# Kernel optimization log

Measured on AMD Instinct MI355X. Metric: run time of the kernel, lower is better.

## Reference

```python
import jax, jax.numpy as jnp
import numpy as np

N, E, B = 8000, 128000, 16
DIN, D, H, C, L = 16, 256, 8, 32, 6
MC, NT = 200, 8
NEG_SLOPE = 0.2


def layernorm(x, s, b):
    mu = jnp.mean(x, axis=-1, keepdims=True)
    var = jnp.mean(jnp.square(x - mu), axis=-1, keepdims=True)
    return (x - mu) * jax.lax.rsqrt(var + 1e-5) * s + b


def setup_inputs() -> dict:
    key = jax.random.key(0)
    ks = iter(jax.random.split(key, 64))
    rn = lambda shape, s=0.05: jax.random.normal(next(ks), shape, jnp.float32) * s
    inp = {}
    inp['x'] = jax.random.normal(next(ks), (N, DIN), jnp.float32)
    inp['edge_index'] = jax.random.randint(next(ks), (2, E), 0, N)
    inp['batch'] = jnp.sort(jax.random.randint(next(ks), (N,), 0, B))
    # node encoder: Linear(DIN,D) + LayerNorm
    inp['enc_W'] = rn((DIN, D)); inp['enc_b'] = jnp.zeros((D,), jnp.float32)
    inp['enc_ls'] = jnp.ones((D,), jnp.float32); inp['enc_lb'] = jnp.zeros((D,), jnp.float32)
    # GATv2 layers (stacked): lin_l, lin_r, att, output bias, post LayerNorm
    inp['Wl'] = rn((L, D, D)); inp['bl'] = jnp.zeros((L, D), jnp.float32)
    inp['Wr'] = rn((L, D, D)); inp['br'] = jnp.zeros((L, D), jnp.float32)
    inp['att'] = rn((L, H, C))
    inp['gb'] = jnp.zeros((L, D), jnp.float32)
    inp['gls'] = jnp.ones((L, D), jnp.float32); inp['glb'] = jnp.zeros((L, D), jnp.float32)
    # color head MLP: D -> D -> D//2 -> MC
    inp['cW1'] = rn((D, D)); inp['cb1'] = jnp.zeros((D,), jnp.float32)
    inp['cW2'] = rn((D, D // 2)); inp['cb2'] = jnp.zeros((D // 2,), jnp.float32)
    inp['cW3'] = rn((D // 2, MC)); inp['cb3'] = jnp.zeros((MC,), jnp.float32)
    # chromatic head: 2D -> D -> D//2 -> MC
    inp['chW1'] = rn((2 * D, D)); inp['chb1'] = jnp.zeros((D,), jnp.float32)
    inp['chW2'] = rn((D, D // 2)); inp['chb2'] = jnp.zeros((D // 2,), jnp.float32)
    inp['chW3'] = rn((D // 2, MC)); inp['chb3'] = jnp.zeros((MC,), jnp.float32)
    # type head: 2D -> 128 -> NT
    inp['tW1'] = rn((2 * D, 128)); inp['tb1'] = jnp.zeros((128,), jnp.float32)
    inp['tW2'] = rn((128, NT)); inp['tb2'] = jnp.zeros((NT,), jnp.float32)
    # difficulty head: 2D -> 64 -> 1, sigmoid * 100
    inp['dW1'] = rn((2 * D, 64)); inp['db1'] = jnp.zeros((64,), jnp.float32)
    inp['dW2'] = rn((64, 1)); inp['db2'] = jnp.zeros((1,), jnp.float32)
    return inp


def reference(x, edge_index, batch, enc_W, enc_b, enc_ls, enc_lb,
              Wl, bl, Wr, br, att, gb, gls, glb,
              cW1, cb1, cW2, cb2, cW3, cb3,
              chW1, chb1, chW2, chb2, chW3, chb3,
              tW1, tb1, tW2, tb2, dW1, db1, dW2, db2):
    n = x.shape[0]
    # node encoder (dropout = identity at inference)
    h = jax.nn.relu(layernorm(x @ enc_W + enc_b, enc_ls, enc_lb))
    # add self loops once (same for every layer)
    sl = jnp.arange(n)
    src = jnp.concatenate([edge_index[0], sl])  # message source j
    dst = jnp.concatenate([edge_index[1], sl])  # message target i
    for i in range(L):
        xl = (h @ Wl[i] + bl[i]).reshape(n, H, C)  # source transform
        xr = (h @ Wr[i] + br[i]).reshape(n, H, C)  # target transform
        # GATv2 attention: a^T LeakyReLU(xl_j + xr_i)
        e = jax.nn.leaky_relu(xl[src] + xr[dst], NEG_SLOPE)  # [E+N, H, C]
        logits = jnp.einsum('ehc,hc->eh', e, att[i])          # [E+N, H]
        # segment softmax over destination node (self-loops guarantee denom > 0)
        m = jax.ops.segment_max(logits, dst, num_segments=n)
        m = jnp.where(jnp.isfinite(m), m, 0.0)
        p = jnp.exp(logits - m[dst])
        denom = jax.ops.segment_sum(p, dst, num_segments=n)
        alpha = p / denom[dst]
        out = jax.ops.segment_sum(xl[src] * alpha[:, :, None], dst, num_segments=n)
        out = out.reshape(n, D) + gb[i]
        h_new = jax.nn.elu(layernorm(out, gls[i], glb[i]))
        h = h + h_new if i > 0 else h_new
    # per-node color logits
    z = jax.nn.relu(h @ cW1 + cb1)
    z = jax.nn.relu(z @ cW2 + cb2)
    node_colors = z @ cW3 + cb3
    # global mean/max pooling per graph
    cnt = jax.ops.segment_sum(jnp.ones((n,), h.dtype), batch, num_segments=B)
    mean_p = jax.ops.segment_sum(h, batch, num_segments=B) / jnp.maximum(cnt, 1.0)[:, None]
    max_p = jax.ops.segment_max(h, batch, num_segments=B)
    max_p = jnp.where(jnp.isfinite(max_p), max_p, 0.0)
    g = jnp.concatenate([mean_p, max_p], axis=1)  # [B, 2D]
    zc = jax.nn.relu(g @ chW1 + chb1)
    zc = jax.nn.relu(zc @ chW2 + chb2)
    chromatic_num = zc @ chW3 + chb3
    zt = jax.nn.relu(g @ tW1 + tb1)
    graph_type = zt @ tW2 + tb2
    zd = jax.nn.relu(g @ dW1 + db1)
    difficulty = jax.nn.sigmoid(zd @ dW2 + db2) * 100.0
    return (node_colors, chromatic_num, graph_type, difficulty)
```

## Files before the change

### kernel.cpp

```cpp
#include <hip/hip_runtime.h>
#include <hip/hip_bf16.h>

constexpr int DIN = 16;
constexpr int D   = 256;
constexpr int NH  = 8;
constexpr int NC  = 32;
constexpr int MC  = 200;
constexpr int NT  = 8;
constexpr int BG  = 16;
constexpr int NL  = 6;
constexpr int PS  = 16;
constexpr float NEG = 0.2f;

typedef __attribute__((ext_vector_type(8))) short bfrag;
typedef __attribute__((ext_vector_type(4))) float f32x4;

__device__ inline unsigned short f2bf(float f) {
    unsigned int u = __float_as_uint(f);
    u += 0x7FFFu + ((u >> 16) & 1u);
    return (unsigned short)(u >> 16);
}
__device__ inline float bf2f(unsigned short u) {
    return __uint_as_float((unsigned int)u << 16);
}

__device__ inline float dot_ilp(const float* __restrict__ g, const float* __restrict__ W,
                                int K, int ldw, int t) {
    float a0 = 0.f, a1 = 0.f, a2 = 0.f, a3 = 0.f;
    for (int k = 0; k < K; k += 4) {
        a0 = fmaf(g[k + 0], W[(k + 0) * ldw + t], a0);
        a1 = fmaf(g[k + 1], W[(k + 1) * ldw + t], a1);
        a2 = fmaf(g[k + 2], W[(k + 2) * ldw + t], a2);
        a3 = fmaf(g[k + 3], W[(k + 3) * ldw + t], a3);
    }
    return (a0 + a1) + (a2 + a3);
}

__global__ __launch_bounds__(256) void init_k(int* __restrict__ deg, int N) {
    int i = blockIdx.x * 256 + threadIdx.x;
    if (i < N) deg[i] = 1;
}

__global__ __launch_bounds__(256) void enc_k(const float* __restrict__ x, const float* __restrict__ W,
                                             const float* __restrict__ b, const float* __restrict__ ls,
                                             const float* __restrict__ lb, float* __restrict__ h, int N) {
    int t = threadIdx.x;
    int lane = t & 63;
    int n = blockIdx.x * 4 + (t >> 6);
    if (n >= N) return;
    int c4 = lane * 4;
    float xs[DIN];
#pragma unroll
    for (int k = 0; k < DIN; k += 4) {
        float4 xv = *(const float4*)&x[n * DIN + k];
        xs[k] = xv.x; xs[k + 1] = xv.y; xs[k + 2] = xv.z; xs[k + 3] = xv.w;
    }
    float4 a = *(const float4*)&b[c4];
#pragma unroll
    for (int k = 0; k < DIN; k++) {
        float4 wv = *(const float4*)&W[k * D + c4];
        a.x = fmaf(xs[k], wv.x, a.x);
        a.y = fmaf(xs[k], wv.y, a.y);
        a.z = fmaf(xs[k], wv.z, a.z);
        a.w = fmaf(xs[k], wv.w, a.w);
    }
    float s = a.x + a.y + a.z + a.w;
#pragma unroll
    for (int msk = 1; msk <= 32; msk <<= 1) s += __shfl_xor(s, msk);
    float mu = s * (1.f / D);
    float4 dv = make_float4(a.x - mu, a.y - mu, a.z - mu, a.w - mu);
    float v2 = dv.x * dv.x + dv.y * dv.y + dv.z * dv.z + dv.w * dv.w;
#pragma unroll
    for (int msk = 1; msk <= 32; msk <<= 1) v2 += __shfl_xor(v2, msk);
    float rstd = rsqrtf(v2 * (1.f / D) + 1e-5f);
    float4 lsv = *(const float4*)&ls[c4];
    float4 lbv = *(const float4*)&lb[c4];
    float4 y = make_float4(fmaxf(dv.x * rstd * lsv.x + lbv.x, 0.f),
                           fmaxf(dv.y * rstd * lsv.y + lbv.y, 0.f),
                           fmaxf(dv.z * rstd * lsv.z + lbv.z, 0.f),
                           fmaxf(dv.w * rstd * lsv.w + lbv.w, 0.f));
    *(float4*)&h[(size_t)n * D + c4] = y;
}

__global__ __launch_bounds__(256) void count_k(const int* __restrict__ dst, int* __restrict__ deg, int E) {
    int e = blockIdx.x * 256 + threadIdx.x;
    if (e < E) atomicAdd(&deg[dst[e]], 1);
}

__global__ __launch_bounds__(1024) void scan_k(const int* __restrict__ deg, int* __restrict__ row_ptr,
                                               int* __restrict__ fill, int N) {
    __shared__ int sd[1024];
    int t = threadIdx.x;
    int chunk = (N + 1023) >> 10;
    int lo = t * chunk, hi = min(lo + chunk, N);
    int s = 0;
    for (int i = lo; i < hi; i++) s += deg[i];
    sd[t] = s;
    __syncthreads();
    for (int off = 1; off < 1024; off <<= 1) {
        int v = (t >= off) ? sd[t - off] : 0;
        __syncthreads();
        sd[t] += v;
        __syncthreads();
    }
    int run = (t > 0) ? sd[t - 1] : 0;
    for (int i = lo; i < hi; i++) {
        row_ptr[i] = run; fill[i] = run;
        run += deg[i];
    }
    if (t == 1023) row_ptr[N] = sd[1023];
}

__global__ __launch_bounds__(256) void scatter_k(const int* __restrict__ src, const int* __restrict__ dst,
                                                 int* __restrict__ fill, int* __restrict__ col, int E, int N) {
    int e = blockIdx.x * 256 + threadIdx.x;
    if (e < E) {
        int p = atomicAdd(&fill[dst[e]], 1);
        col[p] = src[e];
    } else if (e < E + N) {
        int n = e - E;
        int p = atomicAdd(&fill[n], 1);
        col[p] = n;
    }
}

__global__ __launch_bounds__(256) void repack_k(const float* __restrict__ Wl, const float* __restrict__ Wr,
                                                unsigned short* __restrict__ Wp) {
    int tid = blockIdx.x * 256 + threadIdx.x;
    int lane = tid & 63;
    int r1 = tid >> 6;
    int ks = r1 & 7;
    int r2 = r1 >> 3;
    int ct = r2 & 15;
    int mi = r2 >> 4;
    int layer = mi >> 1, mat = mi & 1;
    const float* W = (mat == 0 ? Wl : Wr) + (size_t)layer * D * D;
    int n = ct * 16 + (lane & 15);
    int kb = ks * 32 + (lane >> 4) * 8;
    size_t base = (((size_t)(mi * 16 + ct) * 8 + ks) * 64 + lane) * 8;
#pragma unroll
    for (int j = 0; j < 8; j++) Wp[base + j] = f2bf(W[(size_t)(kb + j) * D + n]);
}

__global__ __launch_bounds__(256) void repack_c(const float* __restrict__ W, unsigned short* __restrict__ Wp,
                                                int K, int NCOL, int nct, int nks) {
    int tid = blockIdx.x * 256 + threadIdx.x;
    int total = nct * nks * 64;
    if (tid >= total) return;
    int lane = tid & 63;
    int r = tid >> 6;
    int ks = r % nks;
    int ct = r / nks;
    int n = ct * 16 + (lane & 15);
    int kb = ks * 32 + (lane >> 4) * 8;
    size_t base = (((size_t)ct * nks + ks) * 64 + lane) * 8;
#pragma unroll
    for (int j = 0; j < 8; j++) {
        int k = kb + j;
        Wp[base + j] = (n < NCOL && k < K) ? f2bf(W[(size_t)k * NCOL + n]) : (unsigned short)0;
    }
}

__global__ __launch_bounds__(256) void gemm_mfma_k(const float* __restrict__ h,
                                                   const unsigned short* __restrict__ WpL,
                                                   const unsigned short* __restrict__ WpR,
                                                   const float* __restrict__ bl, const float* __restrict__ br,
                                                   unsigned short* __restrict__ xl, unsigned short* __restrict__ xr,
                                                   int N) {
    int t = threadIdx.x;
    int lane = t & 63;
    int w = t >> 6;
    int nb = blockIdx.x * 16;
    __shared__ unsigned short As[16][264];
#pragma unroll
    for (int r = 0; r < 16; r++) {
        int row = nb + r;
        float v = (row < N) ? h[(size_t)row * D + t] : 0.f;
        As[r][t] = f2bf(v);
    }
    __syncthreads();
    int m = lane & 15;
    int q = lane >> 4;
    int ctbase = w * 4;
    f32x4 accL[4], accR[4];
#pragma unroll
    for (int ct = 0; ct < 4; ct++) {
        float bLv = bl[(ctbase + ct) * 16 + m];
        float bRv = br[(ctbase + ct) * 16 + m];
        accL[ct] = (f32x4){bLv, bLv, bLv, bLv};
        accR[ct] = (f32x4){bRv, bRv, bRv, bRv};
    }
#pragma unroll 2
    for (int ks = 0; ks < 8; ks++) {
        bfrag af = *(const bfrag*)&As[m][ks * 32 + q * 8];
#pragma unroll
        for (int ct = 0; ct < 4; ct++) {
            int ctg = ctbase + ct;
            size_t off = (((size_t)ctg * 8 + ks) * 64 + lane) * 8;
            bfrag bL = *(const bfrag*)&WpL[off];
            bfrag bR = *(const bfrag*)&WpR[off];
            accL[ct] = __builtin_amdgcn_mfma_f32_16x16x32_bf16(af, bL, accL[ct], 0, 0, 0);
            accR[ct] = __builtin_amdgcn_mfma_f32_16x16x32_bf16(af, bR, accR[ct], 0, 0, 0);
        }
    }
#pragma unroll
    for (int ct = 0; ct < 4; ct++) {
        int colg = (ctbase + ct) * 16 + m;
#pragma unroll
        for (int reg = 0; reg < 4; reg++) {
            int row = nb + q * 4 + reg;
            if (row < N) {
                xl[(size_t)row * D + colg] = f2bf(accL[ct][reg]);
                xr[(size_t)row * D + colg] = f2bf(accR[ct][reg]);
            }
        }
    }
}

__global__ __launch_bounds__(256) void attn_k(const unsigned short* __restrict__ xl,
                                              const unsigned short* __restrict__ xr,
                                              const int* __restrict__ row_ptr, const int* __restrict__ col,
                                              const float* __restrict__ att, const float* __restrict__ gb,
                                              const float* __restrict__ gls, const float* __restrict__ glb,
                                              float* __restrict__ h, int layer, int N) {
    int t = threadIdx.x;
    int lane = t & 63;
    int n = blockIdx.x * 4 + (t >> 6);
    if (n >= N) return;
    int c4 = lane * 4;
    ushort4 xr4 = *(const ushort4*)&xr[(size_t)n * D + c4];
    float4 xrv = make_float4(bf2f(xr4.x), bf2f(xr4.y), bf2f(xr4.z), bf2f(xr4.w));
    float4 av  = *(const float4*)&att[c4];
    int beg = row_ptr[n], end = row_ptr[n + 1];
    int deg = end - beg;
    int myc = col[beg + min(lane, deg - 1)];

    float m = -3.0e38f, l = 0.f;
    float4 acc = make_float4(0.f, 0.f, 0.f, 0.f);

    auto loadx = [&](int i) -> ushort4 {
        if (i < deg) {
            int s = (i < 64) ? __shfl(myc, i) : col[beg + i];
            return *(const ushort4*)&xl[(size_t)s * D + c4];
        }
        return make_ushort4(0, 0, 0, 0);
    };
    auto step = [&](ushort4 x4) {
        float4 xlv = make_float4(bf2f(x4.x), bf2f(x4.y), bf2f(x4.z), bf2f(x4.w));
        float sx = xlv.x + xrv.x; sx = sx > 0.f ? sx : NEG * sx;
        float sy = xlv.y + xrv.y; sy = sy > 0.f ? sy : NEG * sy;
        float sz = xlv.z + xrv.z; sz = sz > 0.f ? sz : NEG * sz;
        float sw = xlv.w + xrv.w; sw = sw > 0.f ? sw : NEG * sw;
        float z = av.x * sx + av.y * sy + av.z * sz + av.w * sw;
        z += __shfl_xor(z, 1); z += __shfl_xor(z, 2); z += __shfl_xor(z, 4);
        float mn = fmaxf(m, z);
        float sc = __expf(m - mn);
        float p  = __expf(z - mn);
        l = l * sc + p;
        acc.x = acc.x * sc + p * xlv.x;
        acc.y = acc.y * sc + p * xlv.y;
        acc.z = acc.z * sc + p * xlv.z;
        acc.w = acc.w * sc + p * xlv.w;
        m = mn;
    };

    ushort4 b0 = loadx(0), b1 = loadx(1), b2 = loadx(2), b3 = loadx(3);
    int e = 0;
    for (; e + 4 <= deg; e += 4) {
        ushort4 n0 = loadx(e + 4), n1 = loadx(e + 5), n2 = loadx(e + 6), n3 = loadx(e + 7);
        step(b0); step(b1); step(b2); step(b3);
        b0 = n0; b1 = n1; b2 = n2; b3 = n3;
    }
    if (e + 0 < deg) step(b0);
    if (e + 1 < deg) step(b1);
    if (e + 2 < deg) step(b2);

    float4 gbv  = *(const float4*)&gb[c4];
    float rl = 1.f / l;
    float4 o = make_float4(acc.x * rl + gbv.x, acc.y * rl + gbv.y,
                           acc.z * rl + gbv.z, acc.w * rl + gbv.w);
    float s = o.x + o.y + o.z + o.w;
#pragma unroll
    for (int msk = 1; msk <= 32; msk <<= 1) s += __shfl_xor(s, msk);
    float mu = s * (1.f / D);
    float4 dv = make_float4(o.x - mu, o.y - mu, o.z - mu, o.w - mu);
    float v2 = dv.x * dv.x + dv.y * dv.y + dv.z * dv.z + dv.w * dv.w;
#pragma unroll
    for (int msk = 1; msk <= 32; msk <<= 1) v2 += __shfl_xor(v2, msk);
    float rstd = rsqrtf(v2 * (1.f / D) + 1e-5f);
    float4 glsv = *(const float4*)&gls[c4];
    float4 glbv = *(const float4*)&glb[c4];
    float y0 = dv.x * rstd * glsv.x + glbv.x;
    float y1 = dv.y * rstd * glsv.y + glbv.y;
    float y2 = dv.z * rstd * glsv.z + glbv.z;
    float y3 = dv.w * rstd * glsv.w + glbv.w;
    y0 = y0 > 0.f ? y0 : expm1f(y0);
    y1 = y1 > 0.f ? y1 : expm1f(y1);
    y2 = y2 > 0.f ? y2 : expm1f(y2);
    y3 = y3 > 0.f ? y3 : expm1f(y3);
    float4 prev = make_float4(0.f, 0.f, 0.f, 0.f);
    if (layer > 0) prev = *(const float4*)&h[(size_t)n * D + c4];
    float4 res = make_float4(prev.x + y0, prev.y + y1, prev.z + y2, prev.w + y3);
    *(float4*)&h[(size_t)n * D + c4] = res;
}

__global__ __launch_bounds__(256) void color_mfma_k(const float* __restrict__ h,
                                                    const unsigned short* __restrict__ W1p, const float* __restrict__ b1,
                                                    const unsigned short* __restrict__ W2p, const float* __restrict__ b2,
                                                    const unsigned short* __restrict__ W3p, const float* __restrict__ b3,
                                                    float* __restrict__ out, int N) {
    int t = threadIdx.x;
    int lane = t & 63;
    int w = t >> 6;
    int nb = blockIdx.x * 16;
    __shared__ unsigned short As[16][264];
    __shared__ unsigned short Zs[16][264];
#pragma unroll
    for (int r = 0; r < 16; r++) {
        int row = nb + r;
        float v = (row < N) ? h[(size_t)row * D + t] : 0.f;
        As[r][t] = f2bf(v);
    }
    __syncthreads();
    int m = lane & 15;
    int q = lane >> 4;
    {
        f32x4 acc[4];
#pragma unroll
        for (int ct = 0; ct < 4; ct++) {
            float bv = b1[(w * 4 + ct) * 16 + m];
            acc[ct] = (f32x4){bv, bv, bv, bv};
        }
#pragma unroll 2
        for (int ks = 0; ks < 8; ks++) {
            bfrag af = *(const bfrag*)&As[m][ks * 32 + q * 8];
#pragma unroll
            for (int ct = 0; ct < 4; ct++) {
                int ctg = w * 4 + ct;
                bfrag bf = *(const bfrag*)&W1p[(((size_t)ctg * 8 + ks) * 64 + lane) * 8];
                acc[ct] = __builtin_amdgcn_mfma_f32_16x16x32_bf16(af, bf, acc[ct], 0, 0, 0);
            }
        }
#pragma unroll
        for (int ct = 0; ct < 4; ct++) {
            int colg = (w * 4 + ct) * 16 + m;
#pragma unroll
            for (int reg = 0; reg < 4; reg++)
                Zs[q * 4 + reg][colg] = f2bf(fmaxf(acc[ct][reg], 0.f));
        }
    }
    __syncthreads();
    {
        f32x4 acc[2];
#pragma unroll
        for (int ct = 0; ct < 2; ct++) {
            float bv = b2[(w * 2 + ct) * 16 + m];
            acc[ct] = (f32x4){bv, bv, bv, bv};
        }
#pragma unroll 2
        for (int ks = 0; ks < 8; ks++) {
            bfrag af = *(const bfrag*)&Zs[m][ks * 32 + q * 8];
#pragma unroll
            for (int ct = 0; ct < 2; ct++) {
                int ctg = w * 2 + ct;
                bfrag bf = *(const bfrag*)&W2p[(((size_t)ctg * 8 + ks) * 64 + lane) * 8];
                acc[ct] = __builtin_amdgcn_mfma_f32_16x16x32_bf16(af, bf, acc[ct], 0, 0, 0);
            }
        }
        __syncthreads();
#pragma unroll
        for (int ct = 0; ct < 2; ct++) {
            int colg = (w * 2 + ct) * 16 + m;
#pragma unroll
            for (int reg = 0; reg < 4; reg++)
                As[q * 4 + reg][colg] = f2bf(fmaxf(acc[ct][reg], 0.f));
        }
    }
    __syncthreads();
    for (int ctg = w; ctg < 13; ctg += 4) {
        int colg = ctg * 16 + m;
        float bv = (colg < MC) ? b3[colg] : 0.f;
        f32x4 acc = (f32x4){bv, bv, bv, bv};
#pragma unroll
        for (int ks = 0; ks < 4; ks++) {
            bfrag af = *(const bfrag*)&As[m][ks * 32 + q * 8];
            bfrag bf = *(const bfrag*)&W3p[(((size_t)ctg * 4 + ks) * 64 + lane) * 8];
            acc = __builtin_amdgcn_mfma_f32_16x16x32_bf16(af, bf, acc, 0, 0, 0);
        }
#pragma unroll
        for (int reg = 0; reg < 4; reg++) {
            int row = nb + q * 4 + reg;
            if (row < N && colg < MC) out[(size_t)row * MC + colg] = acc[reg];
        }
    }
}

__global__ __launch_bounds__(256) void pool_k(const float* __restrict__ h, const int* __restrict__ batch,
                                              float* __restrict__ psum, float* __restrict__ pmax,
                                              int* __restrict__ cnt, int N) {
    int b = blockIdx.x;
    int sl = blockIdx.y;
    int c = threadIdx.x;
    int lo = 0, hi = N;
    while (lo < hi) { int mid = (lo + hi) >> 1; if (batch[mid] < b) lo = mid + 1; else hi = mid; }
    int s0 = lo;
    lo = 0; hi = N;
    while (lo < hi) { int mid = (lo + hi) >> 1; if (batch[mid] < b + 1) lo = mid + 1; else hi = mid; }
    int s1 = lo;
    int len = s1 - s0;
    int chunk = (len + PS - 1) / PS;
    int n0 = s0 + sl * chunk;
    int n1 = min(n0 + chunk, s1);
    float sum = 0.f, mx = -3.0e38f;
    for (int n = n0; n < n1; n++) {
        float v = h[(size_t)n * D + c];
        sum += v;
        mx = fmaxf(mx, v);
    }
    psum[(size_t)(b * PS + sl) * D + c] = sum;
    pmax[(size_t)(b * PS + sl) * D + c] = mx;
    if (c == 0 && sl == 0) cnt[b] = len;
}

__global__ __launch_bounds__(256) void heads_k(const float* __restrict__ psum, const float* __restrict__ pmax,
                                               const int* __restrict__ cnt,
                                               const float* __restrict__ chW1, const float* __restrict__ chb1,
                                               const float* __restrict__ chW2, const float* __restrict__ chb2,
                                               const float* __restrict__ chW3, const float* __restrict__ chb3,
                                               const float* __restrict__ tW1, const float* __restrict__ tb1,
                                               const float* __restrict__ tW2, const float* __restrict__ tb2,
                                               const float* __restrict__ dW1, const float* __restrict__ db1,
                                               const float* __restrict__ dW2, const float* __restrict__ db2,
                                               float* __restrict__ out_ch, float* __restrict__ out_t,
                                               float* __restrict__ out_d) {
    int b = blockIdx.x, sec = blockIdx.y, t = threadIdx.x;
    __shared__ float g[2 * D];
    __shared__ float z1[D];
    __shared__ float z2[128];
    float sum = 0.f, mx = -3.0e38f;
#pragma unroll
    for (int sl = 0; sl < PS; sl++) {
        sum += psum[(size_t)(b * PS + sl) * D + t];
        mx = fmaxf(mx, pmax[(size_t)(b * PS + sl) * D + t]);
    }
    int cn = cnt[b];
    float c = fmaxf((float)cn, 1.f);
    g[t] = sum / c;
    g[D + t] = (cn > 0) ? mx : 0.f;
    __syncthreads();
    if (sec == 0) {
        z1[t] = fmaxf(chb1[t] + dot_ilp(g, chW1, 2 * D, D, t), 0.f);
        __syncthreads();
        if (t < 128) z2[t] = fmaxf(chb2[t] + dot_ilp(z1, chW2, D, 128, t), 0.f);
        __syncthreads();
        if (t < MC) out_ch[b * MC + t] = chb3[t] + dot_ilp(z2, chW3, 128, MC, t);
    } else if (sec == 1) {
        if (t < 128) z1[t] = fmaxf(tb1[t] + dot_ilp(g, tW1, 2 * D, 128, t), 0.f);
        __syncthreads();
        if (t < NT) out_t[b * NT + t] = tb2[t] + dot_ilp(z1, tW2, 128, NT, t);
    } else {
        if (t < 64) z1[t] = fmaxf(db1[t] + dot_ilp(g, dW1, 2 * D, 64, t), 0.f);
        __syncthreads();
        if (t == 0) {
            float a = db2[0] + dot_ilp(z1, dW2, 64, 1, 0);
            out_d[b] = 100.f / (1.f + __expf(-a));
        }
    }
}

extern "C" void kernel_launch(void* const* d_in, const int* in_sizes, int n_in,
                              void* d_out, int out_size, void* d_ws, size_t ws_size,
                              hipStream_t stream) {
    const float* x     = (const float*)d_in[0];
    const int*   ei    = (const int*)d_in[1];
    const int*   batch = (const int*)d_in[2];
    const float* encW  = (const float*)d_in[3];
    const float* encb  = (const float*)d_in[4];
    const float* encls = (const float*)d_in[5];
    const float* enclb = (const float*)d_in[6];
    const float* Wl    = (const float*)d_in[7];
    const float* bl    = (const float*)d_in[8];
    const float* Wr    = (const float*)d_in[9];
    const float* br    = (const float*)d_in[10];
    const float* att   = (const float*)d_in[11];
    const float* gb    = (const float*)d_in[12];
    const float* gls   = (const float*)d_in[13];
    const float* glb   = (const float*)d_in[14];
    const float* cW1   = (const float*)d_in[15];
    const float* cb1   = (const float*)d_in[16];
    const float* cW2   = (const float*)d_in[17];
    const float* cb2   = (const float*)d_in[18];
    const float* cW3   = (const float*)d_in[19];
    const float* cb3   = (const float*)d_in[20];
    const float* chW1  = (const float*)d_in[21];
    const float* chb1  = (const float*)d_in[22];
    const float* chW2  = (const float*)d_in[23];
    const float* chb2  = (const float*)d_in[24];
    const float* chW3  = (const float*)d_in[25];
    const float* chb3  = (const float*)d_in[26];
    const float* tW1   = (const float*)d_in[27];
    const float* tb1   = (const float*)d_in[28];
    const float* tW2   = (const float*)d_in[29];
    const float* tb2   = (const float*)d_in[30];
    const float* dW1   = (const float*)d_in[31];
    const float* db1   = (const float*)d_in[32];
    const float* dW2   = (const float*)d_in[33];
    const float* db2   = (const float*)d_in[34];

    const int N = in_sizes[0] / DIN;
    const int E = in_sizes[1] / 2;
    const int* esrc = ei;
    const int* edst = ei + E;

    char* p = (char*)d_ws;
    auto carve = [&](size_t bytes) { char* r = p; p += (bytes + 255) & ~(size_t)255; return r; };
    int*            row_ptr = (int*)carve((size_t)(N + 1) * 4);
    int*            fill    = (int*)carve((size_t)N * 4);
    int*            deg     = (int*)carve((size_t)N * 4);
    int*            cnt     = (int*)carve((size_t)BG * 4);
    float*          psum    = (float*)carve((size_t)BG * PS * D * 4);
    float*          pmax    = (float*)carve((size_t)BG * PS * D * 4);
    int*            col     = (int*)carve((size_t)(E + N) * 4);
    unsigned short* Wp      = (unsigned short*)carve((size_t)NL * 2 * 65536 * 2);
    unsigned short* cW1p    = (unsigned short*)carve((size_t)16 * 8 * 64 * 8 * 2);
    unsigned short* cW2p    = (unsigned short*)carve((size_t)8 * 8 * 64 * 8 * 2);
    unsigned short* cW3p    = (unsigned short*)carve((size_t)13 * 4 * 64 * 8 * 2);
    float*          h       = (float*)carve((size_t)N * D * 4);
    unsigned short* xl      = (unsigned short*)carve((size_t)N * D * 2);
    unsigned short* xr      = (unsigned short*)carve((size_t)N * D * 2);
    (void)ws_size; (void)n_in; (void)out_size;

    init_k<<<(N + 255) / 256, 256, 0, stream>>>(deg, N);
    enc_k<<<(N + 3) / 4, 256, 0, stream>>>(x, encW, encb, encls, enclb, h, N);
    count_k<<<(E + 255) / 256, 256, 0, stream>>>(edst, deg, E);
    scan_k<<<1, 1024, 0, stream>>>(deg, row_ptr, fill, N);
    scatter_k<<<(E + N + 255) / 256, 256, 0, stream>>>(esrc, edst, fill, col, E, N);
    repack_k<<<384, 256, 0, stream>>>(Wl, Wr, Wp);
    repack_c<<<32, 256, 0, stream>>>(cW1, cW1p, D, D, 16, 8);
    repack_c<<<16, 256, 0, stream>>>(cW2, cW2p, D, 128, 8, 8);
    repack_c<<<13, 256, 0, stream>>>(cW3, cW3p, 128, MC, 13, 4);

    for (int i = 0; i < NL; i++) {
        const unsigned short* WpL = Wp + (size_t)(i * 2 + 0) * 65536;
        const unsigned short* WpR = Wp + (size_t)(i * 2 + 1) * 65536;
        gemm_mfma_k<<<(N + 15) / 16, 256, 0, stream>>>(h, WpL, WpR, bl + i * D, br + i * D, xl, xr, N);
        attn_k<<<(N + 3) / 4, 256, 0, stream>>>(xl, xr, row_ptr, col, att + i * NH * NC,
                                                gb + i * D, gls + i * D, glb + i * D, h, i, N);
    }

    float* out = (float*)d_out;
    color_mfma_k<<<(N + 15) / 16, 256, 0, stream>>>(h, cW1p, cb1, cW2p, cb2, cW3p, cb3, out, N);
    pool_k<<<dim3(BG, PS), 256, 0, stream>>>(h, batch, psum, pmax, cnt, N);
    heads_k<<<dim3(BG, 3), 256, 0, stream>>>(psum, pmax, cnt, chW1, chb1, chW2, chb2, chW3, chb3,
                                             tW1, tb1, tW2, tb2, dW1, db1, dW2, db2,
                                             out + (size_t)N * MC,
                                             out + (size_t)N * MC + BG * MC,
                                             out + (size_t)N * MC + BG * MC + BG * NT);
}
```

Baseline: 489.7 us.

## Fuse each GATv2 attention with next layer's GEMM and merge setup kernels

Each layer's attention/LayerNorm/ELU stage now writes its bf16 result straight into shared memory and runs the next layer's MFMA projection in the same block. The xl/xr buffers are double-buffered so the next layer's projections do not overwrite inputs still being read. The last layer is fused with the color-head MLP. Setup work is merged into fewer kernels: degree init with the encoder, degree counting with all weight repacks, and CSR scatter with the first layer's GEMM. This removes many launches and a reread of h per layer. In exchange, attention now runs on 16-node blocks, so there are fewer blocks and each wave handles four nodes in sequence, which may reduce latency hiding on the irregular gathers.

```diff
diff --git a/kernel.cpp b/kernel.cpp
--- a/kernel.cpp
+++ b/kernel.cpp
@@ -24,8 +24,7 @@
     return __uint_as_float((unsigned int)u << 16);
 }
 
-__device__ inline float dot_ilp(const float* __restrict__ g, const float* __restrict__ W,
-                                int K, int ldw, int t) {
+__device__ inline float dot_ilp(const float* g, const float* __restrict__ W, int K, int ldw, int t) {
     float a0 = 0.f, a1 = 0.f, a2 = 0.f, a3 = 0.f;
     for (int k = 0; k < K; k += 4) {
         a0 = fmaf(g[k + 0], W[(k + 0) * ldw + t], a0);
@@ -36,18 +35,9 @@
     return (a0 + a1) + (a2 + a3);
 }
 
-__global__ __launch_bounds__(256) void init_k(int* __restrict__ deg, int N) {
-    int i = blockIdx.x * 256 + threadIdx.x;
-    if (i < N) deg[i] = 1;
-}
-
-__global__ __launch_bounds__(256) void enc_k(const float* __restrict__ x, const float* __restrict__ W,
-                                             const float* __restrict__ b, const float* __restrict__ ls,
-                                             const float* __restrict__ lb, float* __restrict__ h, int N) {
-    int t = threadIdx.x;
-    int lane = t & 63;
-    int n = blockIdx.x * 4 + (t >> 6);
-    if (n >= N) return;
+
+__device__ inline void enc_node(const float* x, const float* W, const float* b, const float* ls,
+                                const float* lb, float* h, int n, int lane) {
     int c4 = lane * 4;
     float xs[DIN];
 #pragma unroll
@@ -82,151 +72,10 @@
     *(float4*)&h[(size_t)n * D + c4] = y;
 }
 
-__global__ __launch_bounds__(256) void count_k(const int* __restrict__ dst, int* __restrict__ deg, int E) {
-    int e = blockIdx.x * 256 + threadIdx.x;
-    if (e < E) atomicAdd(&deg[dst[e]], 1);
-}
-
-__global__ __launch_bounds__(1024) void scan_k(const int* __restrict__ deg, int* __restrict__ row_ptr,
-                                               int* __restrict__ fill, int N) {
-    __shared__ int sd[1024];
-    int t = threadIdx.x;
-    int chunk = (N + 1023) >> 10;
-    int lo = t * chunk, hi = min(lo + chunk, N);
-    int s = 0;
-    for (int i = lo; i < hi; i++) s += deg[i];
-    sd[t] = s;
-    __syncthreads();
-    for (int off = 1; off < 1024; off <<= 1) {
-        int v = (t >= off) ? sd[t - off] : 0;
-        __syncthreads();
-        sd[t] += v;
-        __syncthreads();
-    }
-    int run = (t > 0) ? sd[t - 1] : 0;
-    for (int i = lo; i < hi; i++) {
-        row_ptr[i] = run; fill[i] = run;
-        run += deg[i];
-    }
-    if (t == 1023) row_ptr[N] = sd[1023];
-}
-
-__global__ __launch_bounds__(256) void scatter_k(const int* __restrict__ src, const int* __restrict__ dst,
-                                                 int* __restrict__ fill, int* __restrict__ col, int E, int N) {
-    int e = blockIdx.x * 256 + threadIdx.x;
-    if (e < E) {
-        int p = atomicAdd(&fill[dst[e]], 1);
-        col[p] = src[e];
-    } else if (e < E + N) {
-        int n = e - E;
-        int p = atomicAdd(&fill[n], 1);
-        col[p] = n;
-    }
-}
-
-__global__ __launch_bounds__(256) void repack_k(const float* __restrict__ Wl, const float* __restrict__ Wr,
-                                                unsigned short* __restrict__ Wp) {
-    int tid = blockIdx.x * 256 + threadIdx.x;
-    int lane = tid & 63;
-    int r1 = tid >> 6;
-    int ks = r1 & 7;
-    int r2 = r1 >> 3;
-    int ct = r2 & 15;
-    int mi = r2 >> 4;
-    int layer = mi >> 1, mat = mi & 1;
-    const float* W = (mat == 0 ? Wl : Wr) + (size_t)layer * D * D;
-    int n = ct * 16 + (lane & 15);
-    int kb = ks * 32 + (lane >> 4) * 8;
-    size_t base = (((size_t)(mi * 16 + ct) * 8 + ks) * 64 + lane) * 8;
-#pragma unroll
-    for (int j = 0; j < 8; j++) Wp[base + j] = f2bf(W[(size_t)(kb + j) * D + n]);
-}
-
-__global__ __launch_bounds__(256) void repack_c(const float* __restrict__ W, unsigned short* __restrict__ Wp,
-                                                int K, int NCOL, int nct, int nks) {
-    int tid = blockIdx.x * 256 + threadIdx.x;
-    int total = nct * nks * 64;
-    if (tid >= total) return;
-    int lane = tid & 63;
-    int r = tid >> 6;
-    int ks = r % nks;
-    int ct = r / nks;
-    int n = ct * 16 + (lane & 15);
-    int kb = ks * 32 + (lane >> 4) * 8;
-    size_t base = (((size_t)ct * nks + ks) * 64 + lane) * 8;
-#pragma unroll
-    for (int j = 0; j < 8; j++) {
-        int k = kb + j;
-        Wp[base + j] = (n < NCOL && k < K) ? f2bf(W[(size_t)k * NCOL + n]) : (unsigned short)0;
-    }
-}
-
-__global__ __launch_bounds__(256) void gemm_mfma_k(const float* __restrict__ h,
-                                                   const unsigned short* __restrict__ WpL,
-                                                   const unsigned short* __restrict__ WpR,
-                                                   const float* __restrict__ bl, const float* __restrict__ br,
-                                                   unsigned short* __restrict__ xl, unsigned short* __restrict__ xr,
-                                                   int N) {
-    int t = threadIdx.x;
-    int lane = t & 63;
-    int w = t >> 6;
-    int nb = blockIdx.x * 16;
-    __shared__ unsigned short As[16][264];
-#pragma unroll
-    for (int r = 0; r < 16; r++) {
-        int row = nb + r;
-        float v = (row < N) ? h[(size_t)row * D + t] : 0.f;
-        As[r][t] = f2bf(v);
-    }
-    __syncthreads();
-    int m = lane & 15;
-    int q = lane >> 4;
-    int ctbase = w * 4;
-    f32x4 accL[4], accR[4];
-#pragma unroll
-    for (int ct = 0; ct < 4; ct++) {
-        float bLv = bl[(ctbase + ct) * 16 + m];
-        float bRv = br[(ctbase + ct) * 16 + m];
-        accL[ct] = (f32x4){bLv, bLv, bLv, bLv};
-        accR[ct] = (f32x4){bRv, bRv, bRv, bRv};
-    }
-#pragma unroll 2
-    for (int ks = 0; ks < 8; ks++) {
-        bfrag af = *(const bfrag*)&As[m][ks * 32 + q * 8];
-#pragma unroll
-        for (int ct = 0; ct < 4; ct++) {
-            int ctg = ctbase + ct;
-            size_t off = (((size_t)ctg * 8 + ks) * 64 + lane) * 8;
-            bfrag bL = *(const bfrag*)&WpL[off];
-            bfrag bR = *(const bfrag*)&WpR[off];
-            accL[ct] = __builtin_amdgcn_mfma_f32_16x16x32_bf16(af, bL, accL[ct], 0, 0, 0);
-            accR[ct] = __builtin_amdgcn_mfma_f32_16x16x32_bf16(af, bR, accR[ct], 0, 0, 0);
-        }
-    }
-#pragma unroll
-    for (int ct = 0; ct < 4; ct++) {
-        int colg = (ctbase + ct) * 16 + m;
-#pragma unroll
-        for (int reg = 0; reg < 4; reg++) {
-            int row = nb + q * 4 + reg;
-            if (row < N) {
-                xl[(size_t)row * D + colg] = f2bf(accL[ct][reg]);
-                xr[(size_t)row * D + colg] = f2bf(accR[ct][reg]);
-            }
-        }
-    }
-}
-
-__global__ __launch_bounds__(256) void attn_k(const unsigned short* __restrict__ xl,
-                                              const unsigned short* __restrict__ xr,
-                                              const int* __restrict__ row_ptr, const int* __restrict__ col,
-                                              const float* __restrict__ att, const float* __restrict__ gb,
-                                              const float* __restrict__ gls, const float* __restrict__ glb,
-                                              float* __restrict__ h, int layer, int N) {
-    int t = threadIdx.x;
-    int lane = t & 63;
-    int n = blockIdx.x * 4 + (t >> 6);
-    if (n >= N) return;
+__device__ inline float4 attn_compute(const unsigned short* xl, const unsigned short* xr,
+                                      const int* row_ptr, const int* col, const float* att,
+                                      const float* gb, const float* gls, const float* glb,
+                                      const float* h, int layer, int n, int lane) {
     int c4 = lane * 4;
     ushort4 xr4 = *(const ushort4*)&xr[(size_t)n * D + c4];
     float4 xrv = make_float4(bf2f(xr4.x), bf2f(xr4.y), bf2f(xr4.z), bf2f(xr4.w));
@@ -234,10 +83,8 @@
     int beg = row_ptr[n], end = row_ptr[n + 1];
     int deg = end - beg;
     int myc = col[beg + min(lane, deg - 1)];
-
     float m = -3.0e38f, l = 0.f;
     float4 acc = make_float4(0.f, 0.f, 0.f, 0.f);
-
     auto loadx = [&](int i) -> ushort4 {
         if (i < deg) {
             int s = (i < 64) ? __shfl(myc, i) : col[beg + i];
@@ -263,7 +110,6 @@
         acc.w = acc.w * sc + p * xlv.w;
         m = mn;
     };
-
     ushort4 b0 = loadx(0), b1 = loadx(1), b2 = loadx(2), b3 = loadx(3);
     int e = 0;
     for (; e + 4 <= deg; e += 4) {
@@ -274,8 +120,7 @@
     if (e + 0 < deg) step(b0);
     if (e + 1 < deg) step(b1);
     if (e + 2 < deg) step(b2);
-
-    float4 gbv  = *(const float4*)&gb[c4];
+    float4 gbv = *(const float4*)&gb[c4];
     float rl = 1.f / l;
     float4 o = make_float4(acc.x * rl + gbv.x, acc.y * rl + gbv.y,
                            acc.z * rl + gbv.z, acc.w * rl + gbv.w);
@@ -300,30 +145,233 @@
     y3 = y3 > 0.f ? y3 : expm1f(y3);
     float4 prev = make_float4(0.f, 0.f, 0.f, 0.f);
     if (layer > 0) prev = *(const float4*)&h[(size_t)n * D + c4];
-    float4 res = make_float4(prev.x + y0, prev.y + y1, prev.z + y2, prev.w + y3);
-    *(float4*)&h[(size_t)n * D + c4] = res;
-}
-
-__global__ __launch_bounds__(256) void color_mfma_k(const float* __restrict__ h,
-                                                    const unsigned short* __restrict__ W1p, const float* __restrict__ b1,
-                                                    const unsigned short* __restrict__ W2p, const float* __restrict__ b2,
-                                                    const unsigned short* __restrict__ W3p, const float* __restrict__ b3,
-                                                    float* __restrict__ out, int N) {
+    return make_float4(prev.x + y0, prev.y + y1, prev.z + y2, prev.w + y3);
+}
+
+__device__ inline void gemm_core(const unsigned short (*As)[264],
+                                 const unsigned short* WpL, const unsigned short* WpR,
+                                 const float* bl, const float* br,
+                                 unsigned short* xl, unsigned short* xr, int N, int nb, int T) {
+    int lane = T & 63, w = T >> 6;
+    int m = lane & 15, q = lane >> 4;
+    int ctbase = w * 4;
+    f32x4 accL[4], accR[4];
+#pragma unroll
+    for (int ct = 0; ct < 4; ct++) {
+        float bLv = bl[(ctbase + ct) * 16 + m];
+        float bRv = br[(ctbase + ct) * 16 + m];
+        accL[ct] = (f32x4){bLv, bLv, bLv, bLv};
+        accR[ct] = (f32x4){bRv, bRv, bRv, bRv};
+    }
+#pragma unroll 2
+    for (int ks = 0; ks < 8; ks++) {
+        bfrag af = *(const bfrag*)&As[m][ks * 32 + q * 8];
+#pragma unroll
+        for (int ct = 0; ct < 4; ct++) {
+            int ctg = ctbase + ct;
+            size_t off = (((size_t)ctg * 8 + ks) * 64 + lane) * 8;
+            bfrag bL = *(const bfrag*)&WpL[off];
+            bfrag bR = *(const bfrag*)&WpR[off];
+            accL[ct] = __builtin_amdgcn_mfma_f32_16x16x32_bf16(af, bL, accL[ct], 0, 0, 0);
+            accR[ct] = __builtin_amdgcn_mfma_f32_16x16x32_bf16(af, bR, accR[ct], 0, 0, 0);
+        }
+    }
+#pragma unroll
+    for (int ct = 0; ct < 4; ct++) {
+        int colg = (ctbase + ct) * 16 + m;
+#pragma unroll
+        for (int reg = 0; reg < 4; reg++) {
+            int row = nb + q * 4 + reg;
+            if (row < N) {
+                xl[(size_t)row * D + colg] = f2bf(accL[ct][reg]);
+                xr[(size_t)row * D + colg] = f2bf(accR[ct][reg]);
+            }
+        }
+    }
+}
+
+__device__ inline void repack_attn_one(const float* Wl, const float* Wr, unsigned short* Wp, int tid) {
+    int lane = tid & 63;
+    int r1 = tid >> 6;
+    int ks = r1 & 7;
+    int r2 = r1 >> 3;
+    int ct = r2 & 15;
+    int mi = r2 >> 4;
+    int layer = mi >> 1, mat = mi & 1;
+    const float* W = (mat == 0 ? Wl : Wr) + (size_t)layer * D * D;
+    int n = ct * 16 + (lane & 15);
+    int kb = ks * 32 + (lane >> 4) * 8;
+    size_t base = (((size_t)(mi * 16 + ct) * 8 + ks) * 64 + lane) * 8;
+#pragma unroll
+    for (int j = 0; j < 8; j++) Wp[base + j] = f2bf(W[(size_t)(kb + j) * D + n]);
+}
+
+__device__ inline void repack_gen_one(const float* W, unsigned short* Wp, int K, int NCOL, int nks, int tid) {
+    int lane = tid & 63;
+    int r = tid >> 6;
+    int ks = r % nks;
+    int ct = r / nks;
+    int n = ct * 16 + (lane & 15);
+    int kb = ks * 32 + (lane >> 4) * 8;
+    size_t base = (((size_t)ct * nks + ks) * 64 + lane) * 8;
+#pragma unroll
+    for (int j = 0; j < 8; j++) {
+        int k = kb + j;
+        Wp[base + j] = (n < NCOL && k < K) ? f2bf(W[(size_t)k * NCOL + n]) : (unsigned short)0;
+    }
+}
+
+
+__global__ __launch_bounds__(256) void init_enc_k(const float* __restrict__ x, const float* __restrict__ W,
+                                                  const float* __restrict__ b, const float* __restrict__ ls,
+                                                  const float* __restrict__ lb, float* __restrict__ h,
+                                                  int* __restrict__ deg, int N) {
+    int gid = blockIdx.x * 256 + threadIdx.x;
+    if (gid < N) deg[gid] = 1;
+    int lane = threadIdx.x & 63;
+    int n = blockIdx.x * 4 + (threadIdx.x >> 6);
+    if (n < N) enc_node(x, W, b, ls, lb, h, n, lane);
+}
+
+__global__ __launch_bounds__(256) void count_repack_k(const int* __restrict__ dst, int* __restrict__ deg, int E,
+                                                      const float* __restrict__ Wl, const float* __restrict__ Wr,
+                                                      unsigned short* __restrict__ Wp,
+                                                      const float* __restrict__ cW1, unsigned short* __restrict__ cW1p,
+                                                      const float* __restrict__ cW2, unsigned short* __restrict__ cW2p,
+                                                      const float* __restrict__ cW3, unsigned short* __restrict__ cW3p) {
+    int gid = blockIdx.x * 256 + threadIdx.x;
+    if (gid < E) atomicAdd(&deg[dst[gid]], 1);
+    if (gid < NL * 2 * 16 * 8 * 64) repack_attn_one(Wl, Wr, Wp, gid);
+    if (gid < 16 * 8 * 64) repack_gen_one(cW1, cW1p, D, D, 8, gid);
+    if (gid < 8 * 8 * 64)  repack_gen_one(cW2, cW2p, D, 128, 8, gid);
+    if (gid < 13 * 4 * 64) repack_gen_one(cW3, cW3p, 128, MC, 4, gid);
+}
+
+__global__ __launch_bounds__(1024) void scan_k(const int* __restrict__ deg, int* __restrict__ row_ptr,
+                                               int* __restrict__ fill, int N) {
+    __shared__ int sd[1024];
     int t = threadIdx.x;
-    int lane = t & 63;
-    int w = t >> 6;
+    int chunk = (N + 1023) >> 10;
+    int lo = t * chunk, hi = min(lo + chunk, N);
+    int s = 0;
+    for (int i = lo; i < hi; i++) s += deg[i];
+    sd[t] = s;
+    __syncthreads();
+    for (int off = 1; off < 1024; off <<= 1) {
+        int v = (t >= off) ? sd[t - off] : 0;
+        __syncthreads();
+        sd[t] += v;
+        __syncthreads();
+    }
+    int run = (t > 0) ? sd[t - 1] : 0;
+    for (int i = lo; i < hi; i++) {
+        row_ptr[i] = run; fill[i] = run;
+        run += deg[i];
+    }
+    if (t == 1023) row_ptr[N] = sd[1023];
+}
+
+__global__ __launch_bounds__(256) void scatter_gemm0_k(const int* __restrict__ src, const int* __restrict__ dst,
+                                                       int* __restrict__ fill, int* __restrict__ col, int E, int N,
+                                                       const float* __restrict__ h,
+                                                       const unsigned short* __restrict__ WpL,
+                                                       const unsigned short* __restrict__ WpR,
+                                                       const float* __restrict__ bl, const float* __restrict__ br,
+                                                       unsigned short* __restrict__ xl, unsigned short* __restrict__ xr) {
+    __shared__ unsigned short As[16][264];
+    int T = threadIdx.x;
+    int tt = blockIdx.x;
+    int ntiles = (N + 15) >> 4;
+    if (tt < ntiles) {
+        int nb = tt * 16;
+#pragma unroll
+        for (int r = 0; r < 16; r++) {
+            int row = nb + r;
+            float v = (row < N) ? h[(size_t)row * D + T] : 0.f;
+            As[r][T] = f2bf(v);
+        }
+        __syncthreads();
+        gemm_core(As, WpL, WpR, bl, br, xl, xr, N, nb, T);
+    }
+    for (int e = blockIdx.x * 256 + T; e < E + N; e += gridDim.x * 256) {
+        if (e < E) {
+            int p = atomicAdd(&fill[dst[e]], 1);
+            col[p] = src[e];
+        } else {
+            int n = e - E;
+            int p = atomicAdd(&fill[n], 1);
+            col[p] = n;
+        }
+    }
+}
+
+__global__ __launch_bounds__(256) void layer_k(const unsigned short* __restrict__ xl_in,
+                                               const unsigned short* __restrict__ xr_in,
+                                               const int* __restrict__ row_ptr, const int* __restrict__ col,
+                                               const float* __restrict__ att, const float* __restrict__ gb,
+                                               const float* __restrict__ gls, const float* __restrict__ glb,
+                                               float* __restrict__ h, int layer, int N,
+                                               const unsigned short* __restrict__ WpL,
+                                               const unsigned short* __restrict__ WpR,
+                                               const float* __restrict__ bl, const float* __restrict__ br,
+                                               unsigned short* __restrict__ xl_out, unsigned short* __restrict__ xr_out) {
+    __shared__ unsigned short As[16][264];
+    int T = threadIdx.x;
+    int lane = T & 63, wv = T >> 6;
     int nb = blockIdx.x * 16;
+    int c4 = lane * 4;
+#pragma unroll
+    for (int r0 = 0; r0 < 4; r0++) {
+        int r = wv * 4 + r0;
+        int n = nb + r;
+        if (n < N) {
+            float4 res = attn_compute(xl_in, xr_in, row_ptr, col, att, gb, gls, glb, h, layer, n, lane);
+            *(float4*)&h[(size_t)n * D + c4] = res;
+            As[r][c4 + 0] = f2bf(res.x);
+            As[r][c4 + 1] = f2bf(res.y);
+            As[r][c4 + 2] = f2bf(res.z);
+            As[r][c4 + 3] = f2bf(res.w);
+        } else {
+            As[r][c4 + 0] = 0; As[r][c4 + 1] = 0; As[r][c4 + 2] = 0; As[r][c4 + 3] = 0;
+        }
+    }
+    __syncthreads();
+    gemm_core(As, WpL, WpR, bl, br, xl_out, xr_out, N, nb, T);
+}
+
+__global__ __launch_bounds__(256) void last_k(const unsigned short* __restrict__ xl_in,
+                                              const unsigned short* __restrict__ xr_in,
+                                              const int* __restrict__ row_ptr, const int* __restrict__ col,
+                                              const float* __restrict__ att, const float* __restrict__ gb,
+                                              const float* __restrict__ gls, const float* __restrict__ glb,
+                                              float* __restrict__ h, int N,
+                                              const unsigned short* __restrict__ W1p, const float* __restrict__ b1,
+                                              const unsigned short* __restrict__ W2p, const float* __restrict__ b2,
+                                              const unsigned short* __restrict__ W3p, const float* __restrict__ b3,
+                                              float* __restrict__ out) {
     __shared__ unsigned short As[16][264];
     __shared__ unsigned short Zs[16][264];
-#pragma unroll
-    for (int r = 0; r < 16; r++) {
-        int row = nb + r;
-        float v = (row < N) ? h[(size_t)row * D + t] : 0.f;
-        As[r][t] = f2bf(v);
+    int T = threadIdx.x;
+    int lane = T & 63, wv = T >> 6;
+    int nb = blockIdx.x * 16;
+    int c4 = lane * 4;
+#pragma unroll
+    for (int r0 = 0; r0 < 4; r0++) {
+        int r = wv * 4 + r0;
+        int n = nb + r;
+        if (n < N) {
+            float4 res = attn_compute(xl_in, xr_in, row_ptr, col, att, gb, gls, glb, h, NL - 1, n, lane);
+            *(float4*)&h[(size_t)n * D + c4] = res;
+            As[r][c4 + 0] = f2bf(res.x);
+            As[r][c4 + 1] = f2bf(res.y);
+            As[r][c4 + 2] = f2bf(res.z);
+            As[r][c4 + 3] = f2bf(res.w);
+        } else {
+            As[r][c4 + 0] = 0; As[r][c4 + 1] = 0; As[r][c4 + 2] = 0; As[r][c4 + 3] = 0;
+        }
     }
     __syncthreads();
-    int m = lane & 15;
-    int q = lane >> 4;
+    int m = lane & 15, q = lane >> 4, w = wv;
     {
         f32x4 acc[4];
 #pragma unroll
@@ -526,30 +574,36 @@
     unsigned short* cW2p    = (unsigned short*)carve((size_t)8 * 8 * 64 * 8 * 2);
     unsigned short* cW3p    = (unsigned short*)carve((size_t)13 * 4 * 64 * 8 * 2);
     float*          h       = (float*)carve((size_t)N * D * 4);
-    unsigned short* xl      = (unsigned short*)carve((size_t)N * D * 2);
-    unsigned short* xr      = (unsigned short*)carve((size_t)N * D * 2);
+    unsigned short* xlA     = (unsigned short*)carve((size_t)N * D * 2);
+    unsigned short* xrA     = (unsigned short*)carve((size_t)N * D * 2);
+    unsigned short* xlB     = (unsigned short*)carve((size_t)N * D * 2);
+    unsigned short* xrB     = (unsigned short*)carve((size_t)N * D * 2);
     (void)ws_size; (void)n_in; (void)out_size;
 
-    init_k<<<(N + 255) / 256, 256, 0, stream>>>(deg, N);
-    enc_k<<<(N + 3) / 4, 256, 0, stream>>>(x, encW, encb, encls, enclb, h, N);
-    count_k<<<(E + 255) / 256, 256, 0, stream>>>(edst, deg, E);
+    const int ntiles = (N + 15) / 16;
+    const int sblocks = max(ntiles, (E + N + 255) / 256);
+
+    init_enc_k<<<(N + 3) / 4, 256, 0, stream>>>(x, encW, encb, encls, enclb, h, deg, N);
+    count_repack_k<<<512, 256, 0, stream>>>(edst, deg, E, Wl, Wr, Wp, cW1, cW1p, cW2, cW2p, cW3, cW3p);
     scan_k<<<1, 1024, 0, stream>>>(deg, row_ptr, fill, N);
-    scatter_k<<<(E + N + 255) / 256, 256, 0, stream>>>(esrc, edst, fill, col, E, N);
-    repack_k<<<384, 256, 0, stream>>>(Wl, Wr, Wp);
-    repack_c<<<32, 256, 0, stream>>>(cW1, cW1p, D, D, 16, 8);
-    repack_c<<<16, 256, 0, stream>>>(cW2, cW2p, D, 128, 8, 8);
-    repack_c<<<13, 256, 0, stream>>>(cW3, cW3p, 128, MC, 13, 4);
-
-    for (int i = 0; i < NL; i++) {
-        const unsigned short* WpL = Wp + (size_t)(i * 2 + 0) * 65536;
-        const unsigned short* WpR = Wp + (size_t)(i * 2 + 1) * 65536;
-        gemm_mfma_k<<<(N + 15) / 16, 256, 0, stream>>>(h, WpL, WpR, bl + i * D, br + i * D, xl, xr, N);
-        attn_k<<<(N + 3) / 4, 256, 0, stream>>>(xl, xr, row_ptr, col, att + i * NH * NC,
-                                                gb + i * D, gls + i * D, glb + i * D, h, i, N);
-    }
-
+    scatter_gemm0_k<<<sblocks, 256, 0, stream>>>(esrc, edst, fill, col, E, N, h,
+                                                 Wp + 0, Wp + (size_t)65536,
+                                                 bl + 0, br + 0, xlA, xrA);
+    for (int l = 0; l < NL - 1; l++) {
+        const unsigned short* xin_l = (l & 1) ? xlB : xlA;
+        const unsigned short* xin_r = (l & 1) ? xrB : xrA;
+        unsigned short* xout_l = (l & 1) ? xlA : xlB;
+        unsigned short* xout_r = (l & 1) ? xrA : xrB;
+        layer_k<<<ntiles, 256, 0, stream>>>(xin_l, xin_r, row_ptr, col, att + l * NH * NC,
+                                            gb + l * D, gls + l * D, glb + l * D, h, l, N,
+                                            Wp + (size_t)((l + 1) * 2 + 0) * 65536,
+                                            Wp + (size_t)((l + 1) * 2 + 1) * 65536,
+                                            bl + (l + 1) * D, br + (l + 1) * D, xout_l, xout_r);
+    }
     float* out = (float*)d_out;
-    color_mfma_k<<<(N + 15) / 16, 256, 0, stream>>>(h, cW1p, cb1, cW2p, cb2, cW3p, cb3, out, N);
+    last_k<<<ntiles, 256, 0, stream>>>(xlB, xrB, row_ptr, col, att + (NL - 1) * NH * NC,
+                                       gb + (NL - 1) * D, gls + (NL - 1) * D, glb + (NL - 1) * D, h, N,
+                                       cW1p, cb1, cW2p, cb2, cW3p, cb3, out);
     pool_k<<<dim3(BG, PS), 256, 0, stream>>>(h, batch, psum, pmax, cnt, N);
     heads_k<<<dim3(BG, 3), 256, 0, stream>>>(psum, pmax, cnt, chW1, chb1, chW2, chb2, chW3, chb3,
                                              tW1, tb1, tW2, tb2, dW1, db1, dW2, db2,
```

Result: slower. 528.7 us (+8.0%).
